# Performance work log

Measured on AMD Instinct MI355X. Metric: run time of the kernel, lower is better.

## Reference

```python
import jax, jax.numpy as jnp
import numpy as np
from jax import lax

INPUT, HIDDEN, OUTPUT = 128, 1024, 128
BATCH, T_STEPS = 256, 512


def _uniform(key, shape, fan_in):
    bound = 1.0 / np.sqrt(fan_in)
    return jax.random.uniform(key, shape, jnp.float32, -bound, bound)


def setup_inputs() -> dict:
    key = jax.random.key(0)
    ks = jax.random.split(key, 7)
    return {
        "x_0": jax.random.normal(ks[0], (BATCH, INPUT), jnp.float32),
        "W_i2h": _uniform(ks[1], (INPUT, HIDDEN), INPUT),
        "b_i2h": _uniform(ks[2], (HIDDEN,), INPUT),
        "W_h2h": _uniform(ks[3], (HIDDEN, HIDDEN), HIDDEN),
        "b_h2h": _uniform(ks[4], (HIDDEN,), HIDDEN),
        "W_h2o": _uniform(ks[5], (HIDDEN, OUTPUT), HIDDEN),
        "b_h2o": _uniform(ks[6], (OUTPUT,), HIDDEN),
        "T": T_STEPS,
    }


def reference(x_0, W_i2h, b_i2h, W_h2h, b_h2h, W_h2o, b_h2o, T):
    batch = x_0.shape[0]
    h0 = jnp.zeros((batch, W_h2h.shape[0]), x_0.dtype)

    def step(carry, _):
        x, h = carry
        # hidden_pre = i2h(x) + h2h(h); hidden = tanh(hidden_pre)
        h = jnp.tanh(x @ W_i2h + b_i2h + h @ W_h2h + b_h2h)
        x_out = h @ W_h2o + b_h2o  # fed back as next input
        return (x_out, h), x_out

    _, ys = lax.scan(step, (x_0, h0), None, length=T - 1)
    # trajectory[0] = x_0, trajectory[t+1] = x_output at step t
    return jnp.concatenate([x_0[None], ys], axis=0)  # [T, B, output]
```

## Files before the change

### kernel.cpp

```cpp
#include <hip/hip_runtime.h>
#include <cstdint>
#include <cstddef>


#define BATCH  256
#define INPUT  128
#define HIDDEN 1024
#define OUTPUT 128
#define TSTEPS 512
#define NCAT   1152
#define NTILE  72
#define GROUPS 16
#define MEMB   16
#define NSLOT  4

#define WS_WFRAG 0u
#define WS_BEFF  2621440u
#define WS_HBUF  2629632u
#define WS_BAR   4726784u
#define BAR_U32S 768

typedef _Float16 f16;
typedef _Float16 v8h __attribute__((ext_vector_type(8)));
typedef float    v4f __attribute__((ext_vector_type(4)));

__device__ __forceinline__ float fast_tanh(float x){
  float e = __expf(2.0f * x);
  return (e - 1.0f) / (e + 1.0f);
}

__global__ void k_bias(const float* __restrict__ bi2h, const float* __restrict__ bh2h,
                       const float* __restrict__ bh2o, const float* __restrict__ Wi2h,
                       float* __restrict__ beff){
  int n = blockIdx.x*256 + threadIdx.x;
  if (n >= 1168) return;
  float v = 0.f;
  if (n < HIDDEN){
    v = bi2h[n] + bh2h[n];
    for (int j=0;j<INPUT;j++) v += bh2o[j]*Wi2h[j*HIDDEN + n];
  } else if (n < NCAT){
    v = bh2o[n - HIDDEN];
  }
  beff[n] = v;
}

__global__ void k_h1(const float* __restrict__ x0, const float* __restrict__ Wi2h,
                     const float* __restrict__ bi2h, const float* __restrict__ bh2h,
                     f16* __restrict__ hbuf){
  int idx = blockIdx.x*256 + threadIdx.x;
  int m = idx >> 10, n = idx & 1023;
  float acc = bi2h[n] + bh2h[n];
  const float* xr = x0 + m*INPUT;
  for (int j=0;j<INPUT;j++) acc += xr[j]*Wi2h[j*HIDDEN + n];
  hbuf[idx] = (f16)fast_tanh(acc);
}

__global__ void k_copy0(const float* __restrict__ x0, float* __restrict__ out){
  int i = blockIdx.x*256 + threadIdx.x;
  out[i] = x0[i];
}

__global__ void k_wfrag(const float* __restrict__ Wh2h, const float* __restrict__ Wh2o,
                        const float* __restrict__ Wi2h, f16* __restrict__ Wfrag){
  int gid = blockIdx.x*256 + threadIdx.x;
  int lane = gid & 63;
  int fi = gid >> 6;
  int c = fi % 5, kk = (fi/5) & 7, wv = (fi/40) & 3, mem = fi/160;
  int k0 = wv*256 + kk*32 + (lane>>4)*8;
  int n  = mem*NTILE + c*16 + (lane & 15);
  f16 vals[8];
  if (n >= NCAT){
    #pragma unroll
    for (int j=0;j<8;j++) vals[j] = (f16)0.f;
  } else if (n >= HIDDEN){
    #pragma unroll
    for (int j=0;j<8;j++) vals[j] = (f16)Wh2o[(k0+j)*OUTPUT + (n-HIDDEN)];
  } else {
    float acc[8];
    #pragma unroll
    for (int j=0;j<8;j++) acc[j] = Wh2h[(k0+j)*HIDDEN + n];
    for (int q=0;q<INPUT;q++){
      float wi = Wi2h[q*HIDDEN + n];
      #pragma unroll
      for (int j=0;j<8;j++) acc[j] += Wh2o[(k0+j)*OUTPUT + q]*wi;
    }
    #pragma unroll
    for (int j=0;j<8;j++) vals[j] = (f16)acc[j];
  }
  v8h pack;
  #pragma unroll
  for (int j=0;j<8;j++) pack[j] = vals[j];
  *(v8h*)(Wfrag + (size_t)gid*8) = pack;
}

__global__ void __launch_bounds__(256, 1)
k_rnn(const f16* __restrict__ Wfrag, const float* __restrict__ beff,
      f16* __restrict__ hbuf, unsigned int* __restrict__ bar,
      float* __restrict__ out){
  extern __shared__ char lds_raw[];
  float*    red    = (float*)lds_raw;
  unsigned* s_slot = (unsigned*)(lds_raw + 16384);

  const int tid  = threadIdx.x;
  const int lane = tid & 63;
  const int wv   = tid >> 6;

  if (tid == 0){
    unsigned xcc;
    asm volatile("s_getreg_b32 %0, hwreg(HW_REG_XCC_ID)" : "=s"(xcc));
    xcc &= 7;
    unsigned slot = atomicAdd(&bar[512 + xcc*32], 1u);
    *s_slot = xcc*32 + (slot & 31u);
  }
  __syncthreads();
  const unsigned sid = *s_slot;
  const int g   = sid >> 4;
  const int mem = sid & 15;
  if (g >= GROUPS) return;
  const int m0   = g * 16;
  const int n0   = mem * NTILE;
  const int quad = lane >> 4;
  const int l15  = lane & 15;

  v8h bw[8][5];
  {
    const f16* wp = Wfrag + ((size_t)((mem*4 + wv)*40)*64 + lane)*8;
    #pragma unroll
    for (int kk=0;kk<8;kk++)
      #pragma unroll
      for (int c=0;c<5;c++)
        bw[kk][c] = *(const v8h*)(wp + (size_t)((kk*5+c)*64)*8);
  }

  float bown[2] = {0.f, 0.f};
  #pragma unroll
  for (int c=0;c<5;c++){
    if ((c & 3) == wv){
      int colT = c*16 + l15;
      int col  = n0 + colT;
      if (colT < NTILE && col < NCAT) bown[c>>2] = beff[col];
    }
  }

  const int kbase = wv*256;
  unsigned int* flg = bar + g*32;

  for (int t=1; t<TSTEPS; ++t){
    if (wv == 0){
      const unsigned target = (unsigned)(t-1);
      unsigned tries = 0;
      for (;;){
        unsigned f = __hip_atomic_load(flg + (lane & 15), __ATOMIC_RELAXED,
                                       __HIP_MEMORY_SCOPE_AGENT);
        if (__all((int)(f >= target))) break;
        if (++tries > 2048u) break;
        __builtin_amdgcn_s_sleep(1);
      }
    }
    __syncthreads();

    const f16* hin  = hbuf + (size_t)((t-1)&(NSLOT-1))*(BATCH*HIDDEN);
    f16*       hout = hbuf + (size_t)(t&(NSLOT-1))*(BATCH*HIDDEN);

    v8h af[8];
    {
      const v8h* abase = (const v8h*)(hin + (size_t)(m0 + l15)*HIDDEN + kbase + quad*8);
      #pragma unroll
      for (int kk=0;kk<8;kk++)
        af[kk] = abase[kk*4];
    }

    v4f acc[5];
    #pragma unroll
    for (int c=0;c<5;c++){ v4f z = {0.f,0.f,0.f,0.f}; acc[c] = z; }

    #pragma unroll
    for (int kk=0;kk<8;kk++){
      #pragma unroll
      for (int c=0;c<5;c++)
        acc[c] = __builtin_amdgcn_mfma_f32_16x16x32_f16(af[kk], bw[kk][c], acc[c], 0,0,0);
    }

    #pragma unroll
    for (int c=0;c<5;c++){
      int owner = c & 3;
      if (wv != owner){
        int rank = (wv > owner) ? wv-1 : wv;
        *(v4f*)(red + ((size_t)(c*3 + rank)*64 + lane)*4) = acc[c];
      }
    }
    __syncthreads();

    #pragma unroll
    for (int c=0;c<5;c++){
      if ((c & 3) == wv){
        int colT = c*16 + l15;
        int col  = n0 + colT;
        if (col < HIDDEN && colT < NTILE){
          v4f s = acc[c];
          #pragma unroll
          for (int r=0;r<3;r++) s += *(const v4f*)(red + ((size_t)(c*3 + r)*64 + lane)*4);
          float b = bown[c>>2];
          #pragma unroll
          for (int r=0;r<4;r++){
            float v = fast_tanh(s[r] + b);
            hout[(size_t)(m0 + quad*4 + r)*HIDDEN + col] = (f16)v;
          }
        }
      }
    }
    __syncthreads();

    if (tid == 0)
      __hip_atomic_store(flg + mem, (unsigned)t, __ATOMIC_RELAXED,
                         __HIP_MEMORY_SCOPE_AGENT);

    #pragma unroll
    for (int c=0;c<5;c++){
      if ((c & 3) == wv){
        int colT = c*16 + l15;
        int col  = n0 + colT;
        if (col >= HIDDEN && colT < NTILE){
          v4f s = acc[c];
          #pragma unroll
          for (int r=0;r<3;r++) s += *(const v4f*)(red + ((size_t)(c*3 + r)*64 + lane)*4);
          float b = bown[c>>2];
          float* op = out + (size_t)t*(BATCH*OUTPUT) + (col - HIDDEN);
          #pragma unroll
          for (int r=0;r<4;r++)
            op[(size_t)(m0 + quad*4 + r)*OUTPUT] = s[r] + b;
        }
      }
    }
  }
}

extern "C" void kernel_launch(void* const* d_in, const int* in_sizes, int n_in,
                              void* d_out, int out_size, void* d_ws, size_t ws_size,
                              hipStream_t stream){
  const float* x0   = (const float*)d_in[0];
  const float* Wi2h = (const float*)d_in[1];
  const float* bi2h = (const float*)d_in[2];
  const float* Wh2h = (const float*)d_in[3];
  const float* bh2h = (const float*)d_in[4];
  const float* Wh2o = (const float*)d_in[5];
  const float* bh2o = (const float*)d_in[6];
  float* out = (float*)d_out;
  char* ws = (char*)d_ws;

  f16*          Wfrag = (f16*)(ws + WS_WFRAG);
  float*        beff  = (float*)(ws + WS_BEFF);
  f16*          hbuf  = (f16*)(ws + WS_HBUF);
  unsigned int* bar   = (unsigned int*)(ws + WS_BAR);

  hipMemsetAsync(bar, 0, BAR_U32S*sizeof(unsigned int), stream);
  k_bias <<<5,    256, 0, stream>>>(bi2h, bh2h, bh2o, Wi2h, beff);
  k_h1   <<<1024, 256, 0, stream>>>(x0, Wi2h, bi2h, bh2h, hbuf);
  k_copy0<<<128,  256, 0, stream>>>(x0, out);
  k_wfrag<<<640,  256, 0, stream>>>(Wh2h, Wh2o, Wi2h, Wfrag);

  hipFuncSetAttribute((const void*)k_rnn, hipFuncAttributeMaxDynamicSharedMemorySize, 98304);
  k_rnn<<<256, 256, 98304, stream>>>(Wfrag, beff, hbuf, bar, out);
}
```

Baseline: 1.530 ms.

## Split K across eight waves per block instead of four

The persistent RNN kernel now launches 512 threads per block. Each of eight waves handles a 128-wide K slice instead of a 256-wide one, and the weight fragment layout is repacked to match. This halves the MFMA chain and the register-resident weights per wave, so each step's latency should drop. The cost is a larger cross-wave LDS reduction (7 partials per column tile) and more waves contending at the block barriers.

```diff
diff --git a/kernel.cpp b/kernel.cpp
--- a/kernel.cpp
+++ b/kernel.cpp
@@ -13,6 +13,9 @@
 #define GROUPS 16
 #define MEMB   16
 #define NSLOT  4
+#define WAVES  8
+#define KSL    128
+#define KCH    4
 
 #define WS_WFRAG 0u
 #define WS_BEFF  2621440u
@@ -65,8 +68,8 @@
   int gid = blockIdx.x*256 + threadIdx.x;
   int lane = gid & 63;
   int fi = gid >> 6;
-  int c = fi % 5, kk = (fi/5) & 7, wv = (fi/40) & 3, mem = fi/160;
-  int k0 = wv*256 + kk*32 + (lane>>4)*8;
+  int c = fi % 5, kk = (fi/5) & 3, wv = (fi/20) & 7, mem = fi/160;
+  int k0 = wv*KSL + kk*32 + (lane>>4)*8;
   int n  = mem*NTILE + c*16 + (lane & 15);
   f16 vals[8];
   if (n >= NCAT){
@@ -93,13 +96,13 @@
   *(v8h*)(Wfrag + (size_t)gid*8) = pack;
 }
 
-__global__ void __launch_bounds__(256, 1)
+__global__ void __launch_bounds__(512, 2)
 k_rnn(const f16* __restrict__ Wfrag, const float* __restrict__ beff,
       f16* __restrict__ hbuf, unsigned int* __restrict__ bar,
       float* __restrict__ out){
   extern __shared__ char lds_raw[];
   float*    red    = (float*)lds_raw;
-  unsigned* s_slot = (unsigned*)(lds_raw + 16384);
+  unsigned* s_slot = (unsigned*)(lds_raw + 36864);
 
   const int tid  = threadIdx.x;
   const int lane = tid & 63;
@@ -122,27 +125,24 @@
   const int quad = lane >> 4;
   const int l15  = lane & 15;
 
-  v8h bw[8][5];
+  v8h bw[KCH][5];
   {
-    const f16* wp = Wfrag + ((size_t)((mem*4 + wv)*40)*64 + lane)*8;
-    #pragma unroll
-    for (int kk=0;kk<8;kk++)
+    const f16* wp = Wfrag + ((size_t)((mem*WAVES + wv)*20)*64 + lane)*8;
+    #pragma unroll
+    for (int kk=0;kk<KCH;kk++)
       #pragma unroll
       for (int c=0;c<5;c++)
         bw[kk][c] = *(const v8h*)(wp + (size_t)((kk*5+c)*64)*8);
   }
 
-  float bown[2] = {0.f, 0.f};
-  #pragma unroll
-  for (int c=0;c<5;c++){
-    if ((c & 3) == wv){
-      int colT = c*16 + l15;
-      int col  = n0 + colT;
-      if (colT < NTILE && col < NCAT) bown[c>>2] = beff[col];
-    }
-  }
-
-  const int kbase = wv*256;
+  float bown = 0.f;
+  if (wv < 5){
+    int colT = wv*16 + l15;
+    int col  = n0 + colT;
+    if (colT < NTILE && col < NCAT) bown = beff[col];
+  }
+
+  const int kbase = wv*KSL;
   unsigned int* flg = bar + g*32;
 
   for (int t=1; t<TSTEPS; ++t){
@@ -162,11 +162,11 @@
     const f16* hin  = hbuf + (size_t)((t-1)&(NSLOT-1))*(BATCH*HIDDEN);
     f16*       hout = hbuf + (size_t)(t&(NSLOT-1))*(BATCH*HIDDEN);
 
-    v8h af[8];
+    v8h af[KCH];
     {
       const v8h* abase = (const v8h*)(hin + (size_t)(m0 + l15)*HIDDEN + kbase + quad*8);
       #pragma unroll
-      for (int kk=0;kk<8;kk++)
+      for (int kk=0;kk<KCH;kk++)
         af[kk] = abase[kk*4];
     }
 
@@ -175,7 +175,7 @@
     for (int c=0;c<5;c++){ v4f z = {0.f,0.f,0.f,0.f}; acc[c] = z; }
 
     #pragma unroll
-    for (int kk=0;kk<8;kk++){
+    for (int kk=0;kk<KCH;kk++){
       #pragma unroll
       for (int c=0;c<5;c++)
         acc[c] = __builtin_amdgcn_mfma_f32_16x16x32_f16(af[kk], bw[kk][c], acc[c], 0,0,0);
@@ -183,29 +183,25 @@
 
     #pragma unroll
     for (int c=0;c<5;c++){
-      int owner = c & 3;
-      if (wv != owner){
-        int rank = (wv > owner) ? wv-1 : wv;
-        *(v4f*)(red + ((size_t)(c*3 + rank)*64 + lane)*4) = acc[c];
+      if (wv != c){
+        int rank = (wv > c) ? wv-1 : wv;
+        *(v4f*)(red + ((size_t)(c*7 + rank)*64 + lane)*4) = acc[c];
       }
     }
     __syncthreads();
 
-    #pragma unroll
-    for (int c=0;c<5;c++){
-      if ((c & 3) == wv){
-        int colT = c*16 + l15;
-        int col  = n0 + colT;
-        if (col < HIDDEN && colT < NTILE){
-          v4f s = acc[c];
-          #pragma unroll
-          for (int r=0;r<3;r++) s += *(const v4f*)(red + ((size_t)(c*3 + r)*64 + lane)*4);
-          float b = bown[c>>2];
-          #pragma unroll
-          for (int r=0;r<4;r++){
-            float v = fast_tanh(s[r] + b);
-            hout[(size_t)(m0 + quad*4 + r)*HIDDEN + col] = (f16)v;
-          }
+    if (wv < 5){
+      const int c = wv;
+      int colT = c*16 + l15;
+      int col  = n0 + colT;
+      if (col < HIDDEN && colT < NTILE){
+        v4f s = acc[c];
+        #pragma unroll
+        for (int r=0;r<7;r++) s += *(const v4f*)(red + ((size_t)(c*7 + r)*64 + lane)*4);
+        #pragma unroll
+        for (int r=0;r<4;r++){
+          float v = fast_tanh(s[r] + bown);
+          hout[(size_t)(m0 + quad*4 + r)*HIDDEN + col] = (f16)v;
         }
       }
     }
@@ -215,21 +211,18 @@
       __hip_atomic_store(flg + mem, (unsigned)t, __ATOMIC_RELAXED,
                          __HIP_MEMORY_SCOPE_AGENT);
 
-    #pragma unroll
-    for (int c=0;c<5;c++){
-      if ((c & 3) == wv){
-        int colT = c*16 + l15;
-        int col  = n0 + colT;
-        if (col >= HIDDEN && colT < NTILE){
-          v4f s = acc[c];
-          #pragma unroll
-          for (int r=0;r<3;r++) s += *(const v4f*)(red + ((size_t)(c*3 + r)*64 + lane)*4);
-          float b = bown[c>>2];
-          float* op = out + (size_t)t*(BATCH*OUTPUT) + (col - HIDDEN);
-          #pragma unroll
-          for (int r=0;r<4;r++)
-            op[(size_t)(m0 + quad*4 + r)*OUTPUT] = s[r] + b;
-        }
+    if (wv < 5){
+      const int c = wv;
+      int colT = c*16 + l15;
+      int col  = n0 + colT;
+      if (col >= HIDDEN && colT < NTILE){
+        v4f s = acc[c];
+        #pragma unroll
+        for (int r=0;r<7;r++) s += *(const v4f*)(red + ((size_t)(c*7 + r)*64 + lane)*4);
+        float* op = out + (size_t)t*(BATCH*OUTPUT) + (col - HIDDEN);
+        #pragma unroll
+        for (int r=0;r<4;r++)
+          op[(size_t)(m0 + quad*4 + r)*OUTPUT] = s[r] + bown;
       }
     }
   }
@@ -260,5 +253,5 @@
   k_wfrag<<<640,  256, 0, stream>>>(Wh2h, Wh2o, Wi2h, Wfrag);
 
   hipFuncSetAttribute((const void*)k_rnn, hipFuncAttributeMaxDynamicSharedMemorySize, 98304);
-  k_rnn<<<256, 256, 98304, stream>>>(Wfrag, beff, hbuf, bar, out);
-}
+  k_rnn<<<256, 512, 98304, stream>>>(Wfrag, beff, hbuf, bar, out);
+}
```

Result: slower. 1.796 ms (+17.4%).
